# Optimization experiments

Hardware: AMD Instinct MI355X
Metric: run time of the kernel (lower is better)

## Reference

```python
import jax, jax.numpy as jnp
import numpy as np

N_NODES = 100000
N_EDGES = 1600000
C = 128
LAYERS = 3
NUM_CLASS = 10
NUM_GRAPHS = 64


def setup_inputs() -> dict:
    key = jax.random.key(0)
    ks = jax.random.split(key, 10)
    s = 1.0 / np.sqrt(C)
    return {
        "x": jax.random.normal(ks[0], (N_NODES, C), dtype=jnp.float32),
        "edge_index": jax.random.randint(ks[1], (2, N_EDGES), 0, N_NODES, dtype=jnp.int64),
        "batch": jnp.sort(jax.random.randint(ks[2], (N_NODES,), 0, NUM_GRAPHS, dtype=jnp.int64)),
        "weight": jax.random.normal(ks[3], (LAYERS, C, C), dtype=jnp.float32) * s,
        "w_ih": jax.random.normal(ks[4], (3 * C, C), dtype=jnp.float32) * s,
        "w_hh": jax.random.normal(ks[5], (3 * C, C), dtype=jnp.float32) * s,
        "b_ih": jax.random.normal(ks[6], (3 * C,), dtype=jnp.float32) * s,
        "b_hh": jax.random.normal(ks[7], (3 * C,), dtype=jnp.float32) * s,
        "lin_w": jax.random.normal(ks[8], (NUM_CLASS, 2 * C), dtype=jnp.float32) * s,
        "lin_b": jax.random.normal(ks[9], (NUM_CLASS,), dtype=jnp.float32) * s,
    }


def _gru_cell(m, h, w_ih, w_hh, b_ih, b_hh):
    # PyTorch GRUCell: gates ordered (r, z, n)
    gi = m @ w_ih.T + b_ih   # [N, 3C]
    gh = h @ w_hh.T + b_hh   # [N, 3C]
    i_r, i_z, i_n = jnp.split(gi, 3, axis=1)
    h_r, h_z, h_n = jnp.split(gh, 3, axis=1)
    r = jax.nn.sigmoid(i_r + h_r)
    z = jax.nn.sigmoid(i_z + h_z)
    n = jnp.tanh(i_n + r * h_n)
    return (1.0 - z) * n + z * h


def reference(x, edge_index, batch, weight, w_ih, w_hh, b_ih, b_hh, lin_w, lin_b):
    src, dst = edge_index[0], edge_index[1]
    n_nodes = x.shape[0]
    h = x
    for i in range(LAYERS):
        m = h @ weight[i]                                  # [N, C]
        # message = x_j (source), aggregated by sum at target
        agg = jax.ops.segment_sum(m[src], dst, num_segments=n_nodes)
        h = _gru_cell(agg, h, w_ih, w_hh, b_ih, b_hh)
    # F.normalize(p=2, dim=1) with eps=1e-12, then ReLU
    norm = jnp.maximum(jnp.linalg.norm(h, axis=1, keepdims=True), 1e-12)
    out = jax.nn.relu(h / norm)
    # global max / mean pool over graphs
    out1 = jax.ops.segment_max(out, batch, num_segments=NUM_GRAPHS)
    sums = jax.ops.segment_sum(out, batch, num_segments=NUM_GRAPHS)
    counts = jax.ops.segment_sum(jnp.ones((n_nodes, 1), out.dtype), batch, num_segments=NUM_GRAPHS)
    out2 = sums / jnp.maximum(counts, 1.0)
    feat = jnp.concatenate([out1, out2], axis=-1)          # [G, 2C]
    return feat @ lin_w.T + lin_b                          # [G, num_class]
```

## Files before the change

### kernel.cpp

```cpp
#include <hip/hip_runtime.h>
#include <hip/hip_bf16.h>

#define THREADS 256
#define POOLS 16
#define BK2LOG 9
#define BK2SZ 512
#define EPT 16
#define CHUNK (EPT * 256)

typedef __attribute__((ext_vector_type(8))) short bf16x8;
typedef __attribute__((ext_vector_type(4))) float f32x4;

static inline size_t align_up(size_t x, size_t a) { return (x + a - 1) & ~(a - 1); }

__device__ __forceinline__ float bf_lo(unsigned v) { return __uint_as_float(v << 16); }
__device__ __forceinline__ float bf_hi(unsigned v) { return __uint_as_float(v & 0xffff0000u); }

__device__ __forceinline__ void gl_lds16(const void* g, void* l) {
  __builtin_amdgcn_global_load_lds(
      (const __attribute__((address_space(1))) unsigned*)g,
      (__attribute__((address_space(3))) unsigned*)l, 16, 0, 0);
}

__global__ void k_detect(const int* __restrict__ ei, int* __restrict__ flag) {
  if (blockIdx.x == 0 && threadIdx.x == 0) {
    int odd_zero = ((ei[1] | ei[3] | ei[5] | ei[7]) == 0);
    int even_nz  = ((ei[0] | ei[2] | ei[4] | ei[6]) != 0);
    flag[0] = (odd_zero && even_nz) ? 1 : 0;
  }
}

__global__ void k_wc(const float* __restrict__ weight, const float* __restrict__ w_ih,
                     float* __restrict__ Wc) {
  int idx = blockIdx.x * blockDim.x + threadIdx.x;
  const int total = 3 * 384 * 128;
  if (idx >= total) return;
  int k = idx & 127;
  int j = (idx >> 7) % 384;
  int i = idx / (384 * 128);
  const float* wp = weight + (size_t)i * (128 * 128) + (size_t)k * 128;
  const float* ip = w_ih + (size_t)j * 128;
  float s = 0.f;
#pragma unroll 8
  for (int t = 0; t < 128; ++t) s += wp[t] * ip[t];
  Wc[idx] = s;
}

__global__ void k_wprep(const float* __restrict__ Wc, const float* __restrict__ whh,
                        __hip_bfloat16* __restrict__ Wp) {
  int idx = blockIdx.x * blockDim.x + threadIdx.x;
  const int per_layer = 8 * 24 * 64 * 8;
  if (idx >= 3 * per_layer) return;
  int layer = idx / per_layer;
  int rem = idx % per_layer;
  int j    = rem & 7;
  int lane = (rem >> 3) & 63;
  int f    = (rem >> 9) % 24;
  int wc   = rem / (24 * 512);
  int col  = wc * 16 + (lane & 15);
  int kl   = (lane >> 4) * 8 + j;
  float v;
  const float* wcl = Wc + (size_t)layer * 384 * 128;
  if (f < 8) {
    int ks = f;
    v = (ks < 4) ? wcl[(size_t)col * 128 + ks * 32 + kl]
                 : whh[(size_t)col * 128 + (ks - 4) * 32 + kl];
  } else if (f < 16) {
    int ks = f - 8;
    v = (ks < 4) ? wcl[(size_t)(128 + col) * 128 + ks * 32 + kl]
                 : whh[(size_t)(128 + col) * 128 + (ks - 4) * 32 + kl];
  } else if (f < 20) {
    int ks = f - 16;
    v = wcl[(size_t)(256 + col) * 128 + ks * 32 + kl];
  } else {
    int ks = f - 20;
    v = whh[(size_t)(256 + col) * 128 + ks * 32 + kl];
  }
  Wp[idx] = __float2bfloat16(v);
}

__global__ void k_init(const float* __restrict__ x, __hip_bfloat16* __restrict__ hb,
                       int total4) {
  int i = blockIdx.x * blockDim.x + threadIdx.x;
  if (i >= total4) return;
  float4 v = ((const float4*)x)[i];
  __hip_bfloat162 a, b;
  a.x = __float2bfloat16(v.x); a.y = __float2bfloat16(v.y);
  b.x = __float2bfloat16(v.z); b.y = __float2bfloat16(v.w);
  ((__hip_bfloat162*)hb)[2 * i]     = a;
  ((__hip_bfloat162*)hb)[2 * i + 1] = b;
}

__global__ void k_bhist(const int* __restrict__ ei, int* __restrict__ bcount,
                        int E, int NB2, const int* __restrict__ flag) {
  __shared__ int lh[256];
  int t = threadIdx.x;
  lh[t] = 0;
  __syncthreads();
  int s64 = flag[0];
  int stride = gridDim.x * blockDim.x;
  for (int i = blockIdx.x * blockDim.x + t; i < E; i += stride) {
    size_t idx = s64 ? 2 * ((size_t)E + (size_t)i) : ((size_t)E + (size_t)i);
    atomicAdd(&lh[ei[idx] >> BK2LOG], 1);
  }
  __syncthreads();
  if (t < NB2 && lh[t]) atomicAdd(&bcount[t], lh[t]);
}

__global__ void k_bscan(const int* __restrict__ bcount, int* __restrict__ boffs,
                        int* __restrict__ bcursor, int NB2, int E) {
  __shared__ int s[256];
  int t = threadIdx.x;
  int v = (t < NB2) ? bcount[t] : 0;
  s[t] = v;
  __syncthreads();
  for (int d = 1; d < 256; d <<= 1) {
    int x = (t >= d) ? s[t - d] : 0;
    __syncthreads();
    s[t] += x;
    __syncthreads();
  }
  if (t < NB2) {
    int o = s[t] - v;
    boffs[t] = o;
    bcursor[t] = o;
  }
  if (t == 0) boffs[NB2] = E;
}

__global__ void k_bscatter(const int* __restrict__ ei, int* __restrict__ bcursor,
                           int* __restrict__ scratch, int E,
                           const int* __restrict__ flag) {
  __shared__ int lcnt[256];
  __shared__ int gbase[256];
  int t = threadIdx.x;
  lcnt[t] = 0;
  __syncthreads();
  int s64 = flag[0];
  int base = blockIdx.x * CHUNK;
  int pk[EPT], bk[EPT];
#pragma unroll
  for (int e = 0; e < EPT; ++e) {
    int i = base + e * 256 + t;
    if (i < E) {
      int sv = ei[s64 ? 2 * (size_t)i : (size_t)i];
      int dv = ei[s64 ? 2 * ((size_t)E + (size_t)i) : ((size_t)E + (size_t)i)];
      bk[e] = dv >> BK2LOG;
      pk[e] = (sv << BK2LOG) | (dv & (BK2SZ - 1));
      atomicAdd(&lcnt[bk[e]], 1);
    } else {
      bk[e] = -1;
    }
  }
  __syncthreads();
  int c = lcnt[t];
  if (c > 0) gbase[t] = atomicAdd(&bcursor[t], c);
  __syncthreads();
  lcnt[t] = 0;
  __syncthreads();
#pragma unroll
  for (int e = 0; e < EPT; ++e) {
    if (bk[e] >= 0) {
      int li = atomicAdd(&lcnt[bk[e]], 1);
      scratch[gbase[bk[e]] + li] = pk[e];
    }
  }
}

__global__ void k_bcsr(const int* __restrict__ scratch, const int* __restrict__ boffs,
                       int* __restrict__ offs, int* __restrict__ csr,
                       int n, int NB2, int E) {
  __shared__ int lcnt[BK2SZ];
  __shared__ int lcur[BK2SZ];
  int b = blockIdx.x, t = threadIdx.x;
  int s = boffs[b], e = boffs[b + 1];
  lcnt[t] = 0;
  lcnt[t + 256] = 0;
  __syncthreads();
  for (int i = s + t; i < e; i += 256)
    atomicAdd(&lcnt[scratch[i] & (BK2SZ - 1)], 1);
  __syncthreads();
  if (t < 64) {
    int run = 0;
    for (int cch = 0; cch < 8; ++cch) {
      int idx = cch * 64 + t;
      int vv = lcnt[idx];
      int inc = vv;
#pragma unroll
      for (int d = 1; d < 64; d <<= 1) {
        int x = __shfl_up(inc, d);
        if (t >= d) inc += x;
      }
      lcur[idx] = run + inc - vv;
      run += __shfl(inc, 63);
    }
  }
  __syncthreads();
  for (int i = t; i < BK2SZ; i += 256) {
    int node = b * BK2SZ + i;
    if (node < n) offs[node] = s + lcur[i];
  }
  if (b == NB2 - 1 && t == 0) offs[n] = E;
  __syncthreads();
  for (int i = s + t; i < e; i += 256) {
    int v = scratch[i];
    int nl = v & (BK2SZ - 1);
    int pos = atomicAdd(&lcur[nl], 1);
    csr[s + pos] = v >> BK2LOG;
  }
}

__global__ void k_bounds(const int* __restrict__ batch, int* __restrict__ gs,
                         int* __restrict__ ge, int n, const int* __restrict__ flag) {
  int i = blockIdx.x * blockDim.x + threadIdx.x;
  if (i >= n) return;
  int s64 = flag[0];
  int b  = batch[s64 ? 2 * (size_t)i : (size_t)i];
  int bp = (i > 0)     ? batch[s64 ? 2 * (size_t)(i - 1) : (size_t)(i - 1)] : -1;
  int bn = (i < n - 1) ? batch[s64 ? 2 * (size_t)(i + 1) : (size_t)(i + 1)] : -1;
  if (i == 0 || bp != b) gs[b] = i;
  if (i == n - 1 || bn != b) ge[b] = i + 1;
}

__global__ void k_agg(const __hip_bfloat16* __restrict__ hb, const int* __restrict__ offs,
                      const int* __restrict__ csr, __hip_bfloat16* __restrict__ agg, int n) {
  int node = (blockIdx.x * THREADS + threadIdx.x) >> 6;
  int lane = threadIdx.x & 63;
  if (node >= n) return;
  const unsigned* base = (const unsigned*)hb + lane;
  int s = offs[node], e = offs[node + 1];
  float ax0 = 0.f, ay0 = 0.f, ax1 = 0.f, ay1 = 0.f;
  float ax2 = 0.f, ay2 = 0.f, ax3 = 0.f, ay3 = 0.f;
  for (int bs = s; bs < e; bs += 64) {
    int cnt = e - bs; if (cnt > 64) cnt = 64;
    int idx = csr[bs + ((lane < cnt) ? lane : (cnt - 1))];
    int j = 0;
    for (; j + 8 <= cnt; j += 8) {
      int s0 = __shfl(idx, j + 0), s1 = __shfl(idx, j + 1);
      int s2 = __shfl(idx, j + 2), s3 = __shfl(idx, j + 3);
      int s4 = __shfl(idx, j + 4), s5 = __shfl(idx, j + 5);
      int s6 = __shfl(idx, j + 6), s7 = __shfl(idx, j + 7);
      unsigned v0 = base[(size_t)s0 * 64], v1 = base[(size_t)s1 * 64];
      unsigned v2 = base[(size_t)s2 * 64], v3 = base[(size_t)s3 * 64];
      unsigned v4 = base[(size_t)s4 * 64], v5 = base[(size_t)s5 * 64];
      unsigned v6 = base[(size_t)s6 * 64], v7 = base[(size_t)s7 * 64];
      ax0 += bf_lo(v0); ay0 += bf_hi(v0); ax1 += bf_lo(v1); ay1 += bf_hi(v1);
      ax2 += bf_lo(v2); ay2 += bf_hi(v2); ax3 += bf_lo(v3); ay3 += bf_hi(v3);
      ax0 += bf_lo(v4); ay0 += bf_hi(v4); ax1 += bf_lo(v5); ay1 += bf_hi(v5);
      ax2 += bf_lo(v6); ay2 += bf_hi(v6); ax3 += bf_lo(v7); ay3 += bf_hi(v7);
    }
    for (; j < cnt; ++j) {
      unsigned v = base[(size_t)__shfl(idx, j) * 64];
      ax0 += bf_lo(v); ay0 += bf_hi(v);
    }
  }
  float ax = (ax0 + ax1) + (ax2 + ax3);
  float ay = (ay0 + ay1) + (ay2 + ay3);
  __hip_bfloat162 o;
  o.x = __float2bfloat16(ax);
  o.y = __float2bfloat16(ay);
  *(__hip_bfloat162*)(agg + (size_t)node * 128 + lane * 2) = o;
}

__launch_bounds__(256, 2)
__global__ void k_gru_pers(const __hip_bfloat16* __restrict__ agg,
                           __hip_bfloat16* __restrict__ hb,
                           const __hip_bfloat16* __restrict__ Wp,
                           const float* __restrict__ b_ih,
                           const float* __restrict__ b_hh,
                           int n, int ntiles) {
  __shared__ __align__(16) __hip_bfloat16 sA[2][2][32 * 128];
  const int t    = threadIdx.x;
  const int lane = t & 63;
  const int wc   = t >> 6;
  const int half = blockIdx.x & 1;
  const int wf   = half * 4 + wc;

  bf16x8 w[24];
  {
    const bf16x8* wp = (const bf16x8*)Wp + (size_t)(wf * 24) * 64 + lane;
#pragma unroll
    for (int f = 0; f < 24; ++f) w[f] = wp[(size_t)f * 64];
  }
  const int col = half * 64 + wc * 16 + (lane & 15);
  const float br  = b_ih[col] + b_hh[col];
  const float bz  = b_ih[128 + col] + b_hh[128 + col];
  const float bin = b_ih[256 + col];
  const float bhn = b_hh[256 + col];

  auto stage = [&](int buf, int tileIdx) {
    const char* ga = (const char*)agg + (size_t)tileIdx * 8192;
    const char* gh = (const char*)hb  + (size_t)tileIdx * 8192;
#pragma unroll
    for (int p = 0; p < 2; ++p) {
      int slot = p * 256 + t;
      int row  = slot >> 4;
      int sc   = (slot & 15) ^ (row & 7);
      int gb   = row * 256 + sc * 16;
      char* la = (char*)&sA[buf][0][0] + p * 4096 + wc * 1024;
      char* lh = (char*)&sA[buf][1][0] + p * 4096 + wc * 1024;
      gl_lds16(ga + gb, la);
      gl_lds16(gh + gb, lh);
    }
  };

  const int tstep = gridDim.x >> 1;
  int tile = blockIdx.x >> 1;
  if (tile < ntiles) stage(0, tile);
  int cur = 0;

  for (; tile < ntiles; tile += tstep) {
    __syncthreads();
    int nxt = tile + tstep;
    if (nxt < ntiles) stage(cur ^ 1, nxt);

    const char* cb = (const char*)&sA[cur][0][0];
    f32x4 ar[2], az[2], ain[2], ahn[2];
#pragma unroll
    for (int mt = 0; mt < 2; ++mt) {
      ar[mt] = (f32x4){0.f, 0.f, 0.f, 0.f};
      az[mt] = (f32x4){0.f, 0.f, 0.f, 0.f};
      ain[mt] = (f32x4){0.f, 0.f, 0.f, 0.f};
      ahn[mt] = (f32x4){0.f, 0.f, 0.f, 0.f};
    }

#pragma unroll
    for (int ks = 0; ks < 4; ++ks) {
      bf16x8 aa[2], ah[2];
#pragma unroll
      for (int mt = 0; mt < 2; ++mt) {
        int row = mt * 16 + (lane & 15);
        int ch  = (ks * 4 + (lane >> 4)) ^ (row & 7);
        aa[mt] = *(const bf16x8*)(cb + row * 256 + ch * 16);
        ah[mt] = *(const bf16x8*)(cb + 8192 + row * 256 + ch * 16);
      }
#pragma unroll
      for (int mt = 0; mt < 2; ++mt) {
        ar[mt]  = __builtin_amdgcn_mfma_f32_16x16x32_bf16(aa[mt], w[ks],      ar[mt], 0, 0, 0);
        ar[mt]  = __builtin_amdgcn_mfma_f32_16x16x32_bf16(ah[mt], w[4 + ks],  ar[mt], 0, 0, 0);
        az[mt]  = __builtin_amdgcn_mfma_f32_16x16x32_bf16(aa[mt], w[8 + ks],  az[mt], 0, 0, 0);
        az[mt]  = __builtin_amdgcn_mfma_f32_16x16x32_bf16(ah[mt], w[12 + ks], az[mt], 0, 0, 0);
        ain[mt] = __builtin_amdgcn_mfma_f32_16x16x32_bf16(aa[mt], w[16 + ks], ain[mt], 0, 0, 0);
        ahn[mt] = __builtin_amdgcn_mfma_f32_16x16x32_bf16(ah[mt], w[20 + ks], ahn[mt], 0, 0, 0);
      }
    }

    const __hip_bfloat16* hbase = &sA[cur][1][0];
    int row0 = tile * 32;
#pragma unroll
    for (int mt = 0; mt < 2; ++mt) {
#pragma unroll
      for (int j = 0; j < 4; ++j) {
        int lr = mt * 16 + (lane >> 4) * 4 + j;
        int grow = row0 + lr;
        if (grow < n) {
          float r  = 1.f / (1.f + __expf(-(ar[mt][j] + br)));
          float z  = 1.f / (1.f + __expf(-(az[mt][j] + bz)));
          float pa = ain[mt][j] + bin + r * (ahn[mt][j] + bhn);
          float e2 = __expf(2.f * pa);
          float nn = 1.f - 2.f / (e2 + 1.f);
          int ch2 = (col >> 3) ^ (lr & 7);
          float hold = __bfloat162float(hbase[lr * 128 + ch2 * 8 + (col & 7)]);
          float o = (1.f - z) * nn + z * hold;
          hb[(size_t)grow * 128 + col] = __float2bfloat16(o);
        }
      }
    }
    cur ^= 1;
  }
}

__global__ void k_norm(const __hip_bfloat16* __restrict__ hb, float* __restrict__ rnorm,
                       int n) {
  int node = (blockIdx.x * THREADS + threadIdx.x) >> 6;
  int lane = threadIdx.x & 63;
  if (node >= n) return;
  unsigned v = ((const unsigned*)hb)[(size_t)node * 64 + lane];
  float a = bf_lo(v), b = bf_hi(v);
  float s = a * a + b * b;
#pragma unroll
  for (int d = 1; d < 64; d <<= 1) s += __shfl_xor(s, d);
  if (lane == 0) rnorm[node] = 1.f / fmaxf(sqrtf(s), 1e-12f);
}

__global__ void k_pool(const __hip_bfloat16* __restrict__ hb, const float* __restrict__ rnorm,
                       const int* __restrict__ gs, const int* __restrict__ ge,
                       float* __restrict__ featp) {
  int g = blockIdx.x, sp = blockIdx.y;
  int c = threadIdx.x;
  int s = gs[g], e = ge[g];
  int len = e - s;
  int chunk = (len + POOLS - 1) / POOLS;
  int ns = s + sp * chunk;
  int ne = ns + chunk; if (ne > e) ne = e;
  float mx = 0.f, sm = 0.f;
  for (int nd = ns; nd < ne; ++nd) {
    float v = __bfloat162float(hb[(size_t)nd * 128 + c]) * rnorm[nd];
    v = fmaxf(v, 0.f);
    mx = fmaxf(mx, v);
    sm += v;
  }
  featp[((size_t)g * POOLS + sp) * 256 + c]       = mx;
  featp[((size_t)g * POOLS + sp) * 256 + 128 + c] = sm;
}

__global__ void k_pool2(const float* __restrict__ featp, const int* __restrict__ gs,
                        const int* __restrict__ ge, float* __restrict__ feat) {
  int g = blockIdx.x;
  int c = threadIdx.x;
  float mx = 0.f, sm = 0.f;
  for (int sp = 0; sp < POOLS; ++sp) {
    float v = featp[((size_t)g * POOLS + sp) * 256 + c];
    mx = fmaxf(mx, v);
    sm += v;
  }
  float cnt = fmaxf((float)(ge[g] - gs[g]), 1.f);
  feat[(size_t)g * 256 + c] = (c < 128) ? mx : (sm / cnt);
}

__global__ void k_final(const float* __restrict__ feat, const float* __restrict__ lin_w,
                        const float* __restrict__ lin_b, float* __restrict__ out) {
  int g = blockIdx.x;
  __shared__ float sf[256];
  sf[threadIdx.x] = feat[(size_t)g * 256 + threadIdx.x];
  __syncthreads();
  if (threadIdx.x < 10) {
    float s = lin_b[threadIdx.x];
    const float* w = lin_w + (size_t)threadIdx.x * 256;
#pragma unroll 8
    for (int c = 0; c < 256; ++c) s += sf[c] * w[c];
    out[(size_t)g * 10 + threadIdx.x] = s;
  }
}

extern "C" void kernel_launch(void* const* d_in, const int* in_sizes, int n_in,
                              void* d_out, int out_size, void* d_ws, size_t ws_size,
                              hipStream_t stream) {
  const float* x      = (const float*)d_in[0];
  const int*   ei     = (const int*)d_in[1];
  const int*   batch  = (const int*)d_in[2];
  const float* weight = (const float*)d_in[3];
  const float* w_ih   = (const float*)d_in[4];
  const float* w_hh   = (const float*)d_in[5];
  const float* b_ih   = (const float*)d_in[6];
  const float* b_hh   = (const float*)d_in[7];
  const float* lin_w  = (const float*)d_in[8];
  const float* lin_b  = (const float*)d_in[9];
  float* out = (float*)d_out;

  const int N = in_sizes[0] / 128;
  const int E = in_sizes[1] / 2;
  const int G = out_size / 10;
  const int NB2 = (N + BK2SZ - 1) / BK2SZ;
  const int WP_PER_LAYER = 8 * 24 * 64 * 8;

  char* wsc = (char*)d_ws;
  size_t off = 0;
  auto take = [&](size_t bytes) -> void* {
    void* p = wsc + off;
    off = align_up(off + bytes, 256);
    return p;
  };
  __hip_bfloat16*  hb     = (__hip_bfloat16*)take((size_t)N * 128 * 2);
  __hip_bfloat16*  agg    = (__hip_bfloat16*)take((size_t)N * 128 * 2);
  float*           Wc     = (float*)take((size_t)3 * 384 * 128 * 4);
  __hip_bfloat16*  Wp     = (__hip_bfloat16*)take((size_t)3 * WP_PER_LAYER * 2);
  float*           rnorm  = (float*)take((size_t)N * 4);
  int*             offs   = (int*)take(((size_t)N + 1) * 4);
  int*             bcount = (int*)take(256 * 4);
  int*             boffs  = (int*)take(257 * 4);
  int*             bcursor= (int*)take(256 * 4);
  int*             csr    = (int*)take((size_t)E * 4);
  int*             gs     = (int*)take((size_t)G * 4);
  int*             ge     = (int*)take((size_t)G * 4);
  float*           featp  = (float*)take((size_t)G * POOLS * 256 * 4);
  float*           feat   = (float*)take((size_t)G * 256 * 4);
  int*             flag   = (int*)take(256);
  int*             scratch = (int*)agg;
  (void)ws_size; (void)n_in;

  hipMemsetAsync(bcount, 0, 256 * 4, stream);
  hipMemsetAsync(gs, 0, (size_t)G * 4, stream);
  hipMemsetAsync(ge, 0, (size_t)G * 4, stream);

  k_detect<<<1, 64, 0, stream>>>(ei, flag);
  k_wc<<<(3 * 384 * 128 + THREADS - 1) / THREADS, THREADS, 0, stream>>>(weight, w_ih, Wc);
  k_wprep<<<(3 * WP_PER_LAYER + THREADS - 1) / THREADS, THREADS, 0, stream>>>(Wc, w_hh, Wp);
  k_init<<<(N * 32 + THREADS - 1) / THREADS, THREADS, 0, stream>>>(x, hb, N * 32);

  k_bhist<<<128, THREADS, 0, stream>>>(ei, bcount, E, NB2, flag);
  k_bscan<<<1, 256, 0, stream>>>(bcount, boffs, bcursor, NB2, E);
  k_bscatter<<<(E + CHUNK - 1) / CHUNK, THREADS, 0, stream>>>(ei, bcursor, scratch, E, flag);
  k_bcsr<<<NB2, THREADS, 0, stream>>>(scratch, boffs, offs, csr, N, NB2, E);
  k_bounds<<<(N + 255) / 256, 256, 0, stream>>>(batch, gs, ge, N, flag);

  const int ntiles = (N + 31) / 32;
  for (int layer = 0; layer < 3; ++layer) {
    k_agg<<<(N + 3) / 4, THREADS, 0, stream>>>(hb, offs, csr, agg, N);
    k_gru_pers<<<512, 256, 0, stream>>>(
        agg, hb, Wp + (size_t)layer * WP_PER_LAYER, b_ih, b_hh, N, ntiles);
  }

  k_norm<<<(N + 3) / 4, THREADS, 0, stream>>>(hb, rnorm, N);
  k_pool<<<dim3(G, POOLS), 128, 0, stream>>>(hb, rnorm, gs, ge, featp);
  k_pool2<<<G, 256, 0, stream>>>(featp, gs, ge, feat);
  k_final<<<G, 256, 0, stream>>>(feat, lin_w, lin_b, out);
}
```

Baseline: 460.8 us.

## Fuse weight prep and pooling kernels, deepen gather unroll, ping-pong hidden state

Merges the weight-combination and weight-packing kernels into one, and merges the pool reduction with the final linear layer, removing two launches and their intermediate buffers. The aggregation gather loop now issues 16 independent loads per batch instead of 8, to keep more memory requests in flight. The GRU kernel reads from one hidden-state buffer and writes to another, which removes aliasing between input and output. Its occupancy hint rises to 3 blocks per CU with a 768-block grid, which may cost registers against the 24 preloaded weight fragments.

```diff
diff --git a/kernel.cpp b/kernel.cpp
--- a/kernel.cpp
+++ b/kernel.cpp
@@ -30,24 +30,8 @@
   }
 }
 
-__global__ void k_wc(const float* __restrict__ weight, const float* __restrict__ w_ih,
-                     float* __restrict__ Wc) {
-  int idx = blockIdx.x * blockDim.x + threadIdx.x;
-  const int total = 3 * 384 * 128;
-  if (idx >= total) return;
-  int k = idx & 127;
-  int j = (idx >> 7) % 384;
-  int i = idx / (384 * 128);
-  const float* wp = weight + (size_t)i * (128 * 128) + (size_t)k * 128;
-  const float* ip = w_ih + (size_t)j * 128;
-  float s = 0.f;
-#pragma unroll 8
-  for (int t = 0; t < 128; ++t) s += wp[t] * ip[t];
-  Wc[idx] = s;
-}
-
-__global__ void k_wprep(const float* __restrict__ Wc, const float* __restrict__ whh,
-                        __hip_bfloat16* __restrict__ Wp) {
+__global__ void k_wcp(const float* __restrict__ weight, const float* __restrict__ w_ih,
+                      const float* __restrict__ whh, __hip_bfloat16* __restrict__ Wp) {
   int idx = blockIdx.x * blockDim.x + threadIdx.x;
   const int per_layer = 8 * 24 * 64 * 8;
   if (idx >= 3 * per_layer) return;
@@ -59,22 +43,24 @@
   int wc   = rem / (24 * 512);
   int col  = wc * 16 + (lane & 15);
   int kl   = (lane >> 4) * 8 + j;
+  int gate, ks;
+  bool from_wc;
+  if (f < 8)       { gate = 0; ks = f;      from_wc = (ks < 4); }
+  else if (f < 16) { gate = 1; ks = f - 8;  from_wc = (ks < 4); }
+  else if (f < 20) { gate = 2; ks = f - 16; from_wc = true;  }
+  else             { gate = 2; ks = f - 20; from_wc = false; }
+  int row = gate * 128 + col;
+  int k   = (ks & 3) * 32 + kl;
   float v;
-  const float* wcl = Wc + (size_t)layer * 384 * 128;
-  if (f < 8) {
-    int ks = f;
-    v = (ks < 4) ? wcl[(size_t)col * 128 + ks * 32 + kl]
-                 : whh[(size_t)col * 128 + (ks - 4) * 32 + kl];
-  } else if (f < 16) {
-    int ks = f - 8;
-    v = (ks < 4) ? wcl[(size_t)(128 + col) * 128 + ks * 32 + kl]
-                 : whh[(size_t)(128 + col) * 128 + (ks - 4) * 32 + kl];
-  } else if (f < 20) {
-    int ks = f - 16;
-    v = wcl[(size_t)(256 + col) * 128 + ks * 32 + kl];
+  if (from_wc) {
+    const float* wp = weight + (size_t)layer * 16384 + (size_t)k * 128;
+    const float* ip = w_ih + (size_t)row * 128;
+    float s = 0.f;
+#pragma unroll 8
+    for (int t = 0; t < 128; ++t) s += wp[t] * ip[t];
+    v = s;
   } else {
-    int ks = f - 20;
-    v = whh[(size_t)(256 + col) * 128 + ks * 32 + kl];
+    v = whh[(size_t)row * 128 + k];
   }
   Wp[idx] = __float2bfloat16(v);
 }
@@ -235,19 +221,28 @@
     int cnt = e - bs; if (cnt > 64) cnt = 64;
     int idx = csr[bs + ((lane < cnt) ? lane : (cnt - 1))];
     int j = 0;
-    for (; j + 8 <= cnt; j += 8) {
-      int s0 = __shfl(idx, j + 0), s1 = __shfl(idx, j + 1);
-      int s2 = __shfl(idx, j + 2), s3 = __shfl(idx, j + 3);
-      int s4 = __shfl(idx, j + 4), s5 = __shfl(idx, j + 5);
-      int s6 = __shfl(idx, j + 6), s7 = __shfl(idx, j + 7);
-      unsigned v0 = base[(size_t)s0 * 64], v1 = base[(size_t)s1 * 64];
-      unsigned v2 = base[(size_t)s2 * 64], v3 = base[(size_t)s3 * 64];
-      unsigned v4 = base[(size_t)s4 * 64], v5 = base[(size_t)s5 * 64];
-      unsigned v6 = base[(size_t)s6 * 64], v7 = base[(size_t)s7 * 64];
-      ax0 += bf_lo(v0); ay0 += bf_hi(v0); ax1 += bf_lo(v1); ay1 += bf_hi(v1);
-      ax2 += bf_lo(v2); ay2 += bf_hi(v2); ax3 += bf_lo(v3); ay3 += bf_hi(v3);
-      ax0 += bf_lo(v4); ay0 += bf_hi(v4); ax1 += bf_lo(v5); ay1 += bf_hi(v5);
-      ax2 += bf_lo(v6); ay2 += bf_hi(v6); ax3 += bf_lo(v7); ay3 += bf_hi(v7);
+    for (; j + 16 <= cnt; j += 16) {
+      unsigned v[16];
+#pragma unroll
+      for (int q = 0; q < 16; ++q)
+        v[q] = base[(size_t)__shfl(idx, j + q) * 64];
+#pragma unroll
+      for (int q = 0; q < 16; q += 4) {
+        ax0 += bf_lo(v[q + 0]); ay0 += bf_hi(v[q + 0]);
+        ax1 += bf_lo(v[q + 1]); ay1 += bf_hi(v[q + 1]);
+        ax2 += bf_lo(v[q + 2]); ay2 += bf_hi(v[q + 2]);
+        ax3 += bf_lo(v[q + 3]); ay3 += bf_hi(v[q + 3]);
+      }
+    }
+    for (; j + 4 <= cnt; j += 4) {
+      unsigned v0 = base[(size_t)__shfl(idx, j + 0) * 64];
+      unsigned v1 = base[(size_t)__shfl(idx, j + 1) * 64];
+      unsigned v2 = base[(size_t)__shfl(idx, j + 2) * 64];
+      unsigned v3 = base[(size_t)__shfl(idx, j + 3) * 64];
+      ax0 += bf_lo(v0); ay0 += bf_hi(v0);
+      ax1 += bf_lo(v1); ay1 += bf_hi(v1);
+      ax2 += bf_lo(v2); ay2 += bf_hi(v2);
+      ax3 += bf_lo(v3); ay3 += bf_hi(v3);
     }
     for (; j < cnt; ++j) {
       unsigned v = base[(size_t)__shfl(idx, j) * 64];
@@ -262,9 +257,10 @@
   *(__hip_bfloat162*)(agg + (size_t)node * 128 + lane * 2) = o;
 }
 
-__launch_bounds__(256, 2)
+__launch_bounds__(256, 3)
 __global__ void k_gru_pers(const __hip_bfloat16* __restrict__ agg,
-                           __hip_bfloat16* __restrict__ hb,
+                           const __hip_bfloat16* __restrict__ hin,
+                           __hip_bfloat16* __restrict__ hout,
                            const __hip_bfloat16* __restrict__ Wp,
                            const float* __restrict__ b_ih,
                            const float* __restrict__ b_hh,
@@ -290,7 +286,7 @@
 
   auto stage = [&](int buf, int tileIdx) {
     const char* ga = (const char*)agg + (size_t)tileIdx * 8192;
-    const char* gh = (const char*)hb  + (size_t)tileIdx * 8192;
+    const char* gh = (const char*)hin + (size_t)tileIdx * 8192;
 #pragma unroll
     for (int p = 0; p < 2; ++p) {
       int slot = p * 256 + t;
@@ -362,7 +358,7 @@
           int ch2 = (col >> 3) ^ (lr & 7);
           float hold = __bfloat162float(hbase[lr * 128 + ch2 * 8 + (col & 7)]);
           float o = (1.f - z) * nn + z * hold;
-          hb[(size_t)grow * 128 + col] = __float2bfloat16(o);
+          hout[(size_t)grow * 128 + col] = __float2bfloat16(o);
         }
       }
     }
@@ -404,10 +400,12 @@
   featp[((size_t)g * POOLS + sp) * 256 + 128 + c] = sm;
 }
 
-__global__ void k_pool2(const float* __restrict__ featp, const int* __restrict__ gs,
-                        const int* __restrict__ ge, float* __restrict__ feat) {
+__global__ void k_pool2f(const float* __restrict__ featp, const int* __restrict__ gs,
+                         const int* __restrict__ ge, const float* __restrict__ lin_w,
+                         const float* __restrict__ lin_b, float* __restrict__ out) {
   int g = blockIdx.x;
   int c = threadIdx.x;
+  __shared__ float sf[256];
   float mx = 0.f, sm = 0.f;
   for (int sp = 0; sp < POOLS; ++sp) {
     float v = featp[((size_t)g * POOLS + sp) * 256 + c];
@@ -415,21 +413,14 @@
     sm += v;
   }
   float cnt = fmaxf((float)(ge[g] - gs[g]), 1.f);
-  feat[(size_t)g * 256 + c] = (c < 128) ? mx : (sm / cnt);
-}
-
-__global__ void k_final(const float* __restrict__ feat, const float* __restrict__ lin_w,
-                        const float* __restrict__ lin_b, float* __restrict__ out) {
-  int g = blockIdx.x;
-  __shared__ float sf[256];
-  sf[threadIdx.x] = feat[(size_t)g * 256 + threadIdx.x];
-  __syncthreads();
-  if (threadIdx.x < 10) {
-    float s = lin_b[threadIdx.x];
-    const float* w = lin_w + (size_t)threadIdx.x * 256;
+  sf[c] = (c < 128) ? mx : (sm / cnt);
+  __syncthreads();
+  if (c < 10) {
+    float s = lin_b[c];
+    const float* w = lin_w + (size_t)c * 256;
 #pragma unroll 8
-    for (int c = 0; c < 256; ++c) s += sf[c] * w[c];
-    out[(size_t)g * 10 + threadIdx.x] = s;
+    for (int k = 0; k < 256; ++k) s += sf[k] * w[k];
+    out[(size_t)g * 10 + c] = s;
   }
 }
 
@@ -461,9 +452,9 @@
     off = align_up(off + bytes, 256);
     return p;
   };
-  __hip_bfloat16*  hb     = (__hip_bfloat16*)take((size_t)N * 128 * 2);
+  __hip_bfloat16*  hb0    = (__hip_bfloat16*)take((size_t)N * 128 * 2);
+  __hip_bfloat16*  hb1    = (__hip_bfloat16*)take((size_t)N * 128 * 2);
   __hip_bfloat16*  agg    = (__hip_bfloat16*)take((size_t)N * 128 * 2);
-  float*           Wc     = (float*)take((size_t)3 * 384 * 128 * 4);
   __hip_bfloat16*  Wp     = (__hip_bfloat16*)take((size_t)3 * WP_PER_LAYER * 2);
   float*           rnorm  = (float*)take((size_t)N * 4);
   int*             offs   = (int*)take(((size_t)N + 1) * 4);
@@ -474,7 +465,6 @@
   int*             gs     = (int*)take((size_t)G * 4);
   int*             ge     = (int*)take((size_t)G * 4);
   float*           featp  = (float*)take((size_t)G * POOLS * 256 * 4);
-  float*           feat   = (float*)take((size_t)G * 256 * 4);
   int*             flag   = (int*)take(256);
   int*             scratch = (int*)agg;
   (void)ws_size; (void)n_in;
@@ -484,9 +474,9 @@
   hipMemsetAsync(ge, 0, (size_t)G * 4, stream);
 
   k_detect<<<1, 64, 0, stream>>>(ei, flag);
-  k_wc<<<(3 * 384 * 128 + THREADS - 1) / THREADS, THREADS, 0, stream>>>(weight, w_ih, Wc);
-  k_wprep<<<(3 * WP_PER_LAYER + THREADS - 1) / THREADS, THREADS, 0, stream>>>(Wc, w_hh, Wp);
-  k_init<<<(N * 32 + THREADS - 1) / THREADS, THREADS, 0, stream>>>(x, hb, N * 32);
+  k_wcp<<<(3 * WP_PER_LAYER + THREADS - 1) / THREADS, THREADS, 0, stream>>>(
+      weight, w_ih, w_hh, Wp);
+  k_init<<<(N * 32 + THREADS - 1) / THREADS, THREADS, 0, stream>>>(x, hb0, N * 32);
 
   k_bhist<<<128, THREADS, 0, stream>>>(ei, bcount, E, NB2, flag);
   k_bscan<<<1, 256, 0, stream>>>(bcount, boffs, bcursor, NB2, E);
@@ -495,14 +485,16 @@
   k_bounds<<<(N + 255) / 256, 256, 0, stream>>>(batch, gs, ge, N, flag);
 
   const int ntiles = (N + 31) / 32;
+  __hip_bfloat16* hin = hb0;
+  __hip_bfloat16* hout = hb1;
   for (int layer = 0; layer < 3; ++layer) {
-    k_agg<<<(N + 3) / 4, THREADS, 0, stream>>>(hb, offs, csr, agg, N);
-    k_gru_pers<<<512, 256, 0, stream>>>(
-        agg, hb, Wp + (size_t)layer * WP_PER_LAYER, b_ih, b_hh, N, ntiles);
-  }
-
-  k_norm<<<(N + 3) / 4, THREADS, 0, stream>>>(hb, rnorm, N);
-  k_pool<<<dim3(G, POOLS), 128, 0, stream>>>(hb, rnorm, gs, ge, featp);
-  k_pool2<<<G, 256, 0, stream>>>(featp, gs, ge, feat);
-  k_final<<<G, 256, 0, stream>>>(feat, lin_w, lin_b, out);
-}
+    k_agg<<<(N + 3) / 4, THREADS, 0, stream>>>(hin, offs, csr, agg, N);
+    k_gru_pers<<<768, 256, 0, stream>>>(
+        agg, hin, hout, Wp + (size_t)layer * WP_PER_LAYER, b_ih, b_hh, N, ntiles);
+    __hip_bfloat16* tmp = hin; hin = hout; hout = tmp;
+  }
+
+  k_norm<<<(N + 3) / 4, THREADS, 0, stream>>>(hin, rnorm, N);
+  k_pool<<<dim3(G, POOLS), 128, 0, stream>>>(hin, rnorm, gs, ge, featp);
+  k_pool2f<<<G, 256, 0, stream>>>(featp, gs, ge, lin_w, lin_b, out);
+}
```

Measured after the change: 493.0 us. 1.07x slower.
